# Optimization experiments

Hardware: AMD Instinct MI355X
Metric: run time of the kernel (lower is better)

Reference implementation:

```python
import jax, jax.numpy as jnp
import numpy as np

N_NODES = 100000
N_EDGES = 1600000
IN_DIM, HIDDEN, OUT = 128, 64, 32


def setup_inputs() -> dict:
    key = jax.random.key(0)
    k1, k2, k3, k4 = jax.random.split(key, 4)
    x = jax.random.normal(k1, (N_NODES, IN_DIM), dtype=jnp.float32)
    edge_index = jax.random.randint(k2, (2, N_EDGES), 0, N_NODES, dtype=jnp.int64)
    # Glorot-style init for GCN weights
    W1 = jax.random.normal(k3, (IN_DIM, HIDDEN), dtype=jnp.float32) / np.sqrt(IN_DIM)
    b1 = jnp.zeros((HIDDEN,), dtype=jnp.float32)
    W2 = jax.random.normal(k4, (HIDDEN, OUT), dtype=jnp.float32) / np.sqrt(HIDDEN)
    b2 = jnp.zeros((OUT,), dtype=jnp.float32)
    return {"x": x, "edge_index": edge_index, "W1": W1, "b1": b1, "W2": W2, "b2": b2}


def _gcn_conv(x, src, dst, W, b, n_nodes):
    """PyG GCNConv: h = W x; symmetric-normalized scatter-add over edges
    (self-loops already appended to src/dst)."""
    h = x @ W  # [N, F_out] — transform first (F_out <= F_in)
    ones = jnp.ones_like(dst, dtype=h.dtype)
    deg = jax.ops.segment_sum(ones, dst, num_segments=n_nodes)  # in-degree incl. self-loop
    dinv = jnp.where(deg > 0, jax.lax.rsqrt(deg), 0.0)
    norm = dinv[src] * dinv[dst]  # [E]
    msg = h[src] * norm[:, None]  # [E, F_out] — dominant gather
    agg = jax.ops.segment_sum(msg, dst, num_segments=n_nodes)  # [N, F_out]
    return agg + b


def reference(x, edge_index, W1, b1, W2, b2):
    n_nodes = x.shape[0]
    loops = jnp.arange(n_nodes, dtype=edge_index.dtype)
    src = jnp.concatenate([edge_index[0], loops])
    dst = jnp.concatenate([edge_index[1], loops])
    h = jax.nn.relu(_gcn_conv(x, src, dst, W1, b1, n_nodes))
    out = jax.nn.relu(_gcn_conv(h, src, dst, W2, b2, n_nodes))
    return out
```

## Files before the change

### kernel.cpp

```cpp
#include <hip/hip_runtime.h>

#define IN_DIM 128
#define HID    64
#define OUTD   32

#define BSHIFT 9
#define BNODES 512
#define NB     196
#define BCAP   16384
#define CHUNK  4096

#define XPAD   136

typedef __attribute__((ext_vector_type(8))) short bf16x8;
typedef __attribute__((ext_vector_type(4))) float f32x4;


__device__ __forceinline__ unsigned bfp2(float x, float y) {
    unsigned a = __float_as_uint(x); a = a + 0x7FFF + ((a >> 16) & 1);
    unsigned b = __float_as_uint(y); b = b + 0x7FFF + ((b >> 16) & 1);
    return (a >> 16) | (b & 0xFFFF0000u);
}

__device__ __forceinline__ unsigned short bf1(float x) {
    unsigned u = __float_as_uint(x);
    u += 0x7FFF + ((u >> 16) & 1);
    return (unsigned short)(u >> 16);
}

__device__ __forceinline__ void acc8(float* f, uint4 q) {
    f[0] += __uint_as_float(q.x << 16); f[1] += __uint_as_float(q.x & 0xFFFF0000u);
    f[2] += __uint_as_float(q.y << 16); f[3] += __uint_as_float(q.y & 0xFFFF0000u);
    f[4] += __uint_as_float(q.z << 16); f[5] += __uint_as_float(q.z & 0xFFFF0000u);
    f[6] += __uint_as_float(q.w << 16); f[7] += __uint_as_float(q.w & 0xFFFF0000u);
}


__global__ void k_binit(int* __restrict__ bucketCursor) {
    int t = threadIdx.x;
    if (t < NB) bucketCursor[t] = t * BCAP;
}


__launch_bounds__(256)
__global__ void k_bscatter(const int* __restrict__ src, const int* __restrict__ dst,
                           int* __restrict__ bucketCursor, int* __restrict__ ebuf, int E) {
    __shared__ int h[NB];
    __shared__ int lbase[NB];
    __shared__ int lcur[NB];
    const int t = threadIdx.x;
    const int base = blockIdx.x * CHUNK;
    const int nI4 = (min(CHUNK, E - base)) >> 2;
    const int4* d4 = (const int4*)(dst + base);
    const int4* s4 = (const int4*)(src + base);

    int4 dv0, dv1, dv2, dv3;
    const bool v0 = t < nI4, v1 = t + 256 < nI4, v2 = t + 512 < nI4, v3 = t + 768 < nI4;
    if (v0) dv0 = d4[t];
    if (v1) dv1 = d4[t + 256];
    if (v2) dv2 = d4[t + 512];
    if (v3) dv3 = d4[t + 768];

    for (int i = t; i < NB; i += 256) { h[i] = 0; lcur[i] = 0; }
    __syncthreads();

    if (v0) { atomicAdd(&h[dv0.x >> BSHIFT], 1); atomicAdd(&h[dv0.y >> BSHIFT], 1);
              atomicAdd(&h[dv0.z >> BSHIFT], 1); atomicAdd(&h[dv0.w >> BSHIFT], 1); }
    if (v1) { atomicAdd(&h[dv1.x >> BSHIFT], 1); atomicAdd(&h[dv1.y >> BSHIFT], 1);
              atomicAdd(&h[dv1.z >> BSHIFT], 1); atomicAdd(&h[dv1.w >> BSHIFT], 1); }
    if (v2) { atomicAdd(&h[dv2.x >> BSHIFT], 1); atomicAdd(&h[dv2.y >> BSHIFT], 1);
              atomicAdd(&h[dv2.z >> BSHIFT], 1); atomicAdd(&h[dv2.w >> BSHIFT], 1); }
    if (v3) { atomicAdd(&h[dv3.x >> BSHIFT], 1); atomicAdd(&h[dv3.y >> BSHIFT], 1);
              atomicAdd(&h[dv3.z >> BSHIFT], 1); atomicAdd(&h[dv3.w >> BSHIFT], 1); }
    __syncthreads();

    for (int i = t; i < NB; i += 256)
        lbase[i] = h[i] ? atomicAdd(&bucketCursor[i], h[i]) : 0;
    __syncthreads();

    #define SC1(D, S) { int b_ = (D) >> BSHIFT; int off_ = atomicAdd(&lcur[b_], 1); \
                        ebuf[lbase[b_] + off_] = ((S) << BSHIFT) | ((D) & (BNODES - 1)); }
    if (v0) { int4 sv = s4[t];       SC1(dv0.x, sv.x); SC1(dv0.y, sv.y); SC1(dv0.z, sv.z); SC1(dv0.w, sv.w); }
    if (v1) { int4 sv = s4[t + 256]; SC1(dv1.x, sv.x); SC1(dv1.y, sv.y); SC1(dv1.z, sv.z); SC1(dv1.w, sv.w); }
    if (v2) { int4 sv = s4[t + 512]; SC1(dv2.x, sv.x); SC1(dv2.y, sv.y); SC1(dv2.z, sv.z); SC1(dv2.w, sv.w); }
    if (v3) { int4 sv = s4[t + 768]; SC1(dv3.x, sv.x); SC1(dv3.y, sv.y); SC1(dv3.z, sv.z); SC1(dv3.w, sv.w); }
    #undef SC1
}


__launch_bounds__(256)
__global__ void k_bfinal(const int* __restrict__ ebuf, const int* __restrict__ bucketCursor,
                         int* __restrict__ rs, int* __restrict__ re, float* __restrict__ dinv,
                         int* __restrict__ csr, int N) {
    __shared__ int hist[BNODES];
    __shared__ int rsl[BNODES];
    __shared__ int ssum[256];
    const int t = threadIdx.x;
    const int b = blockIdx.x;
    const int nodeBase = b << BSHIFT;
    const int ebase = b * BCAP;
    const int cnt = bucketCursor[b] - ebase;
    const int nI4 = cnt >> 2;
    const int4* e4 = (const int4*)(ebuf + ebase);

    hist[t] = 0; hist[t + 256] = 0;
    __syncthreads();
    for (int i = t; i < nI4; i += 256) {
        int4 v = e4[i];
        atomicAdd(&hist[v.x & (BNODES - 1)], 1);
        atomicAdd(&hist[v.y & (BNODES - 1)], 1);
        atomicAdd(&hist[v.z & (BNODES - 1)], 1);
        atomicAdd(&hist[v.w & (BNODES - 1)], 1);
    }
    if (t < (cnt & 3))
        atomicAdd(&hist[ebuf[ebase + (nI4 << 2) + t] & (BNODES - 1)], 1);
    __syncthreads();

    int h0 = hist[2 * t], h1 = hist[2 * t + 1];
    ssum[t] = h0 + h1;
    __syncthreads();
    for (int off = 1; off < 256; off <<= 1) {
        int u = (t >= off) ? ssum[t - off] : 0;
        __syncthreads();
        ssum[t] += u;
        __syncthreads();
    }
    int excl = ssum[t] - h0 - h1;
    rsl[2 * t]     = excl;
    rsl[2 * t + 1] = excl + h0;

    int n0 = nodeBase + 2 * t, n1 = n0 + 1;
    if (n0 < N) {
        rs[n0] = ebase + excl;           re[n0] = ebase + excl + h0;
        dinv[n0] = rsqrtf((float)h0 + 1.0f);
    }
    if (n1 < N) {
        rs[n1] = ebase + excl + h0;      re[n1] = ebase + excl + h0 + h1;
        dinv[n1] = rsqrtf((float)h1 + 1.0f);
    }

    hist[2 * t] = 0; hist[2 * t + 1] = 0;
    __syncthreads();

    #define FILL1(P) { int l_ = (P) & (BNODES - 1); int off_ = atomicAdd(&hist[l_], 1); \
                       csr[ebase + rsl[l_] + off_] = ((unsigned)(P)) >> BSHIFT; }
    for (int i = t; i < nI4; i += 256) {
        int4 v = e4[i];
        FILL1(v.x); FILL1(v.y); FILL1(v.z); FILL1(v.w);
    }
    if (t < (cnt & 3))
        FILL1(ebuf[ebase + (nI4 << 2) + t]);
    #undef FILL1
}


__launch_bounds__(256)
__global__ void k_gemm1(const float* __restrict__ x, const float* __restrict__ W1,
                        const float* __restrict__ dinv, unsigned short* __restrict__ hs1b, int N) {
    __shared__ unsigned short xsb[64 * XPAD];
    __shared__ unsigned short wsb[64 * XPAD];
    const int t = threadIdx.x;
    const int base = blockIdx.x * 64;

    for (int i = t; i < IN_DIM * HID; i += 256) {
        int k = i >> 6, n = i & 63;
        wsb[n * XPAD + k] = bf1(W1[i]);
    }
    {
        const float4* s4 = (const float4*)(x + (size_t)base * IN_DIM);
        #pragma unroll
        for (int j = 0; j < 8; ++j) {
            int idx = t + j * 256;
            int r = idx >> 5, k4 = (idx & 31) * 4;
            ushort4 o;
            if (base + r < N) {
                float4 v = s4[idx];
                o.x = bf1(v.x); o.y = bf1(v.y); o.z = bf1(v.z); o.w = bf1(v.w);
            } else {
                o.x = 0; o.y = 0; o.z = 0; o.w = 0;
            }
            *(ushort4*)&xsb[r * XPAD + k4] = o;
        }
    }
    __syncthreads();

    const int lane = t & 63;
    const int w    = t >> 6;
    const int lr   = lane & 15;
    const int kg   = lane >> 4;

    f32x4 acc0 = {0,0,0,0}, acc1 = {0,0,0,0}, acc2 = {0,0,0,0}, acc3 = {0,0,0,0};
    #pragma unroll
    for (int kb = 0; kb < 4; ++kb) {
        int ko = kb * 32 + kg * 8;
        bf16x8 af = *(const bf16x8*)&xsb[(w * 16 + lr) * XPAD + ko];
        bf16x8 b0 = *(const bf16x8*)&wsb[( 0 + lr) * XPAD + ko];
        bf16x8 b1 = *(const bf16x8*)&wsb[(16 + lr) * XPAD + ko];
        bf16x8 b2 = *(const bf16x8*)&wsb[(32 + lr) * XPAD + ko];
        bf16x8 b3 = *(const bf16x8*)&wsb[(48 + lr) * XPAD + ko];
        acc0 = __builtin_amdgcn_mfma_f32_16x16x32_bf16(af, b0, acc0, 0, 0, 0);
        acc1 = __builtin_amdgcn_mfma_f32_16x16x32_bf16(af, b1, acc1, 0, 0, 0);
        acc2 = __builtin_amdgcn_mfma_f32_16x16x32_bf16(af, b2, acc2, 0, 0, 0);
        acc3 = __builtin_amdgcn_mfma_f32_16x16x32_bf16(af, b3, acc3, 0, 0, 0);
    }

    #pragma unroll
    for (int j = 0; j < 4; ++j) {
        int node = base + w * 16 + kg * 4 + j;
        if (node < N) {
            float d = dinv[node];
            unsigned short* o = hs1b + (size_t)node * HID + lr;
            o[0]  = bf1(acc0[j] * d);
            o[16] = bf1(acc1[j] * d);
            o[32] = bf1(acc2[j] * d);
            o[48] = bf1(acc3[j] * d);
        }
    }
}


__launch_bounds__(128)
__global__ void k_fuse2(const uint4* __restrict__ hs, const int* __restrict__ rs,
                        const int* __restrict__ re, const int* __restrict__ csr,
                        const float* __restrict__ dinv,
                        const float* __restrict__ b1, const float* __restrict__ W2,
                        uint2* __restrict__ hs2b, int N) {
    __shared__ float Ws[HID * OUTD];
    __shared__ float L1s[16 * 68];
    const int t = threadIdx.x;
    const int base = blockIdx.x * 16;

    for (int i = t; i < HID * OUTD / 4; i += 128)
        ((float4*)Ws)[i] = ((const float4*)W2)[i];

    {
        int node = base + (t >> 3);
        int lane = t & 7;
        float fa[8] = {0,0,0,0,0,0,0,0};
        float fb[8] = {0,0,0,0,0,0,0,0};
        float fc[8] = {0,0,0,0,0,0,0,0};
        float fd[8] = {0,0,0,0,0,0,0,0};
        acc8(fa, hs[(size_t)node * 8 + lane]);
        int i = rs[node];
        const int end = re[node];
        for (; i + 4 <= end; i += 4) {
            int s0 = __builtin_nontemporal_load(csr + i);
            int s1 = __builtin_nontemporal_load(csr + i + 1);
            int s2 = __builtin_nontemporal_load(csr + i + 2);
            int s3 = __builtin_nontemporal_load(csr + i + 3);
            uint4 q0 = hs[(size_t)s0 * 8 + lane];
            uint4 q1 = hs[(size_t)s1 * 8 + lane];
            uint4 q2 = hs[(size_t)s2 * 8 + lane];
            uint4 q3 = hs[(size_t)s3 * 8 + lane];
            acc8(fa, q0); acc8(fb, q1); acc8(fc, q2); acc8(fd, q3);
        }
        if (i + 2 <= end) {
            int s0 = __builtin_nontemporal_load(csr + i);
            int s1 = __builtin_nontemporal_load(csr + i + 1);
            uint4 q0 = hs[(size_t)s0 * 8 + lane];
            uint4 q1 = hs[(size_t)s1 * 8 + lane];
            acc8(fa, q0); acc8(fb, q1);
            i += 2;
        }
        if (i < end) {
            int s0 = __builtin_nontemporal_load(csr + i);
            acc8(fa, hs[(size_t)s0 * 8 + lane]);
        }
        float dn = dinv[node];
        const float4* bb4 = (const float4*)(b1 + lane * 8);
        float4 bv0 = bb4[0], bv1 = bb4[1];
        float* Lrow = &L1s[(t >> 3) * 68 + lane * 8];
        Lrow[0] = fmaxf((fa[0] + fb[0] + fc[0] + fd[0]) * dn + bv0.x, 0.0f);
        Lrow[1] = fmaxf((fa[1] + fb[1] + fc[1] + fd[1]) * dn + bv0.y, 0.0f);
        Lrow[2] = fmaxf((fa[2] + fb[2] + fc[2] + fd[2]) * dn + bv0.z, 0.0f);
        Lrow[3] = fmaxf((fa[3] + fb[3] + fc[3] + fd[3]) * dn + bv0.w, 0.0f);
        Lrow[4] = fmaxf((fa[4] + fb[4] + fc[4] + fd[4]) * dn + bv1.x, 0.0f);
        Lrow[5] = fmaxf((fa[5] + fb[5] + fc[5] + fd[5]) * dn + bv1.y, 0.0f);
        Lrow[6] = fmaxf((fa[6] + fb[6] + fc[6] + fd[6]) * dn + bv1.z, 0.0f);
        Lrow[7] = fmaxf((fa[7] + fb[7] + fc[7] + fd[7]) * dn + bv1.w, 0.0f);
    }
    __syncthreads();

    {
        const int fq = t & 7;
        const int nl = t >> 3;
        float4 a = {0,0,0,0};
        #pragma unroll 8
        for (int k = 0; k < HID; ++k) {
            float4 w = ((const float4*)Ws)[k * 8 + fq];
            float xv = L1s[nl * 68 + k];
            a.x += xv * w.x; a.y += xv * w.y; a.z += xv * w.z; a.w += xv * w.w;
        }
        int n = base + nl;
        float d = dinv[n];
        a.x *= d; a.y *= d; a.z *= d; a.w *= d;
        hs2b[(size_t)n * 8 + fq] = make_uint2(bfp2(a.x, a.y), bfp2(a.z, a.w));
    }
}


__launch_bounds__(128)
__global__ void k_agg2(const uint4* __restrict__ hs, const int* __restrict__ rs,
                       const int* __restrict__ re, const int* __restrict__ csr,
                       const float* __restrict__ dinv,
                       const float* __restrict__ b2, float* __restrict__ out, int N) {
    int tid = blockIdx.x * 128 + threadIdx.x;
    int node = tid >> 2;
    int lane = tid & 3;

    float fa[8] = {0,0,0,0,0,0,0,0};
    float fb[8] = {0,0,0,0,0,0,0,0};
    float fc[8] = {0,0,0,0,0,0,0,0};
    float fd[8] = {0,0,0,0,0,0,0,0};
    acc8(fa, hs[(size_t)node * 4 + lane]);
    int i = rs[node];
    const int end = re[node];
    for (; i + 4 <= end; i += 4) {
        int s0 = __builtin_nontemporal_load(csr + i);
        int s1 = __builtin_nontemporal_load(csr + i + 1);
        int s2 = __builtin_nontemporal_load(csr + i + 2);
        int s3 = __builtin_nontemporal_load(csr + i + 3);
        uint4 q0 = hs[(size_t)s0 * 4 + lane];
        uint4 q1 = hs[(size_t)s1 * 4 + lane];
        uint4 q2 = hs[(size_t)s2 * 4 + lane];
        uint4 q3 = hs[(size_t)s3 * 4 + lane];
        acc8(fa, q0); acc8(fb, q1); acc8(fc, q2); acc8(fd, q3);
    }
    if (i + 2 <= end) {
        int s0 = __builtin_nontemporal_load(csr + i);
        int s1 = __builtin_nontemporal_load(csr + i + 1);
        uint4 q0 = hs[(size_t)s0 * 4 + lane];
        uint4 q1 = hs[(size_t)s1 * 4 + lane];
        acc8(fa, q0); acc8(fb, q1);
        i += 2;
    }
    if (i < end) {
        int s0 = __builtin_nontemporal_load(csr + i);
        acc8(fa, hs[(size_t)s0 * 4 + lane]);
    }
    float dn = dinv[node];
    const float4* bb4 = (const float4*)(b2 + lane * 8);
    float4 b0 = bb4[0], b1v = bb4[1];
    float4 o0, o1;
    o0.x = fmaxf((fa[0] + fb[0] + fc[0] + fd[0]) * dn + b0.x, 0.0f);
    o0.y = fmaxf((fa[1] + fb[1] + fc[1] + fd[1]) * dn + b0.y, 0.0f);
    o0.z = fmaxf((fa[2] + fb[2] + fc[2] + fd[2]) * dn + b0.z, 0.0f);
    o0.w = fmaxf((fa[3] + fb[3] + fc[3] + fd[3]) * dn + b0.w, 0.0f);
    o1.x = fmaxf((fa[4] + fb[4] + fc[4] + fd[4]) * dn + b1v.x, 0.0f);
    o1.y = fmaxf((fa[5] + fb[5] + fc[5] + fd[5]) * dn + b1v.y, 0.0f);
    o1.z = fmaxf((fa[6] + fb[6] + fc[6] + fd[6]) * dn + b1v.z, 0.0f);
    o1.w = fmaxf((fa[7] + fb[7] + fc[7] + fd[7]) * dn + b1v.w, 0.0f);
    float4* o = (float4*)(out + (size_t)node * OUTD + lane * 8);
    o[0] = o0;
    o[1] = o1;
}


extern "C" void kernel_launch(void* const* d_in, const int* in_sizes, int n_in,
                              void* d_out, int out_size, void* d_ws, size_t ws_size,
                              hipStream_t stream) {
    const float* x  = (const float*)d_in[0];
    const int*   ei = (const int*)  d_in[1];
    const float* W1 = (const float*)d_in[2];
    const float* b1 = (const float*)d_in[3];
    const float* W2 = (const float*)d_in[4];
    const float* b2 = (const float*)d_in[5];

    const int N = in_sizes[0] / IN_DIM;
    const int E = in_sizes[1] / 2;
    const int* srcI = ei;
    const int* dstI = ei + E;
    float* out = (float*)d_out;

    float* dinv         = (float*)d_ws;
    int*   rs           = (int*)d_ws + 131072;
    int*   re           = (int*)d_ws + 2 * 131072;
    int*   bucketCursor = (int*)d_ws + 3 * 131072;
    int*   ebuf         = (int*)d_ws + 4 * 131072;
    int*   csr          = ebuf + (size_t)NB * BCAP;
    uint2* hs1b         = (uint2*)(csr + (size_t)NB * BCAP);
    uint2* hs2b         = hs1b + (size_t)N * 16;

    k_binit   <<<1, 256, 0, stream>>>(bucketCursor);
    k_bscatter<<<(E + CHUNK - 1) / CHUNK, 256, 0, stream>>>(srcI, dstI, bucketCursor, ebuf, E);
    k_bfinal  <<<NB, 256, 0, stream>>>(ebuf, bucketCursor, rs, re, dinv, csr, N);

    k_gemm1<<<(N + 63) / 64, 256, 0, stream>>>(x, W1, dinv, (unsigned short*)hs1b, N);
    k_fuse2<<<N / 16, 128, 0, stream>>>((const uint4*)hs1b, rs, re, csr, dinv, b1, W2, hs2b, N);
    k_agg2 <<<N / 32, 128, 0, stream>>>((const uint4*)hs2b, rs, re, csr, dinv, b2, out, N);
}
```

Before: 128.2 us.

## Co-schedule layer-1 GEMM with edge bucket scatter in one launch

The first-layer GEMM no longer depends on dinv, so it is merged into the bucket-scatter kernel as extra blocks, letting the dense transform overlap with the edge bucketing. The source-side normalization moves into the layer-1 aggregation, which now gathers dinv[src] per edge and uses an FMA instead of an add. The intent is to remove a dependent launch and hide GEMM time behind the atomic-heavy scatter. In exchange, each edge costs an extra random 4-byte gather, and the merged kernel's larger shared-memory footprint may lower occupancy for the scatter blocks.

```diff
diff --git a/kernel.cpp b/kernel.cpp
--- a/kernel.cpp
+++ b/kernel.cpp
@@ -35,6 +35,17 @@
     f[6] += __uint_as_float(q.w << 16); f[7] += __uint_as_float(q.w & 0xFFFF0000u);
 }
 
+__device__ __forceinline__ void facc8(float* f, uint4 q, float s) {
+    f[0] = fmaf(__uint_as_float(q.x << 16),          s, f[0]);
+    f[1] = fmaf(__uint_as_float(q.x & 0xFFFF0000u),  s, f[1]);
+    f[2] = fmaf(__uint_as_float(q.y << 16),          s, f[2]);
+    f[3] = fmaf(__uint_as_float(q.y & 0xFFFF0000u),  s, f[3]);
+    f[4] = fmaf(__uint_as_float(q.z << 16),          s, f[4]);
+    f[5] = fmaf(__uint_as_float(q.z & 0xFFFF0000u),  s, f[5]);
+    f[6] = fmaf(__uint_as_float(q.w << 16),          s, f[6]);
+    f[7] = fmaf(__uint_as_float(q.w & 0xFFFF0000u),  s, f[7]);
+}
+
 
 __global__ void k_binit(int* __restrict__ bucketCursor) {
     int t = threadIdx.x;
@@ -43,48 +54,111 @@
 
 
 __launch_bounds__(256)
-__global__ void k_bscatter(const int* __restrict__ src, const int* __restrict__ dst,
-                           int* __restrict__ bucketCursor, int* __restrict__ ebuf, int E) {
+__global__ void k_bsg(const int* __restrict__ src, const int* __restrict__ dst,
+                      int* __restrict__ bucketCursor, int* __restrict__ ebuf, int E, int nBsc,
+                      const float* __restrict__ x, const float* __restrict__ W1,
+                      unsigned short* __restrict__ hs1b, int N) {
     __shared__ int h[NB];
     __shared__ int lbase[NB];
     __shared__ int lcur[NB];
+    __shared__ unsigned short xsb[64 * XPAD];
+    __shared__ unsigned short wsb[64 * XPAD];
     const int t = threadIdx.x;
-    const int base = blockIdx.x * CHUNK;
-    const int nI4 = (min(CHUNK, E - base)) >> 2;
-    const int4* d4 = (const int4*)(dst + base);
-    const int4* s4 = (const int4*)(src + base);
-
-    int4 dv0, dv1, dv2, dv3;
-    const bool v0 = t < nI4, v1 = t + 256 < nI4, v2 = t + 512 < nI4, v3 = t + 768 < nI4;
-    if (v0) dv0 = d4[t];
-    if (v1) dv1 = d4[t + 256];
-    if (v2) dv2 = d4[t + 512];
-    if (v3) dv3 = d4[t + 768];
-
-    for (int i = t; i < NB; i += 256) { h[i] = 0; lcur[i] = 0; }
-    __syncthreads();
-
-    if (v0) { atomicAdd(&h[dv0.x >> BSHIFT], 1); atomicAdd(&h[dv0.y >> BSHIFT], 1);
-              atomicAdd(&h[dv0.z >> BSHIFT], 1); atomicAdd(&h[dv0.w >> BSHIFT], 1); }
-    if (v1) { atomicAdd(&h[dv1.x >> BSHIFT], 1); atomicAdd(&h[dv1.y >> BSHIFT], 1);
-              atomicAdd(&h[dv1.z >> BSHIFT], 1); atomicAdd(&h[dv1.w >> BSHIFT], 1); }
-    if (v2) { atomicAdd(&h[dv2.x >> BSHIFT], 1); atomicAdd(&h[dv2.y >> BSHIFT], 1);
-              atomicAdd(&h[dv2.z >> BSHIFT], 1); atomicAdd(&h[dv2.w >> BSHIFT], 1); }
-    if (v3) { atomicAdd(&h[dv3.x >> BSHIFT], 1); atomicAdd(&h[dv3.y >> BSHIFT], 1);
-              atomicAdd(&h[dv3.z >> BSHIFT], 1); atomicAdd(&h[dv3.w >> BSHIFT], 1); }
-    __syncthreads();
-
-    for (int i = t; i < NB; i += 256)
-        lbase[i] = h[i] ? atomicAdd(&bucketCursor[i], h[i]) : 0;
-    __syncthreads();
-
-    #define SC1(D, S) { int b_ = (D) >> BSHIFT; int off_ = atomicAdd(&lcur[b_], 1); \
-                        ebuf[lbase[b_] + off_] = ((S) << BSHIFT) | ((D) & (BNODES - 1)); }
-    if (v0) { int4 sv = s4[t];       SC1(dv0.x, sv.x); SC1(dv0.y, sv.y); SC1(dv0.z, sv.z); SC1(dv0.w, sv.w); }
-    if (v1) { int4 sv = s4[t + 256]; SC1(dv1.x, sv.x); SC1(dv1.y, sv.y); SC1(dv1.z, sv.z); SC1(dv1.w, sv.w); }
-    if (v2) { int4 sv = s4[t + 512]; SC1(dv2.x, sv.x); SC1(dv2.y, sv.y); SC1(dv2.z, sv.z); SC1(dv2.w, sv.w); }
-    if (v3) { int4 sv = s4[t + 768]; SC1(dv3.x, sv.x); SC1(dv3.y, sv.y); SC1(dv3.z, sv.z); SC1(dv3.w, sv.w); }
-    #undef SC1
+
+    if ((int)blockIdx.x < nBsc) {
+        const int base = blockIdx.x * CHUNK;
+        const int nI4 = (min(CHUNK, E - base)) >> 2;
+        const int4* d4 = (const int4*)(dst + base);
+        const int4* s4 = (const int4*)(src + base);
+
+        int4 dv0, dv1, dv2, dv3;
+        const bool v0 = t < nI4, v1 = t + 256 < nI4, v2 = t + 512 < nI4, v3 = t + 768 < nI4;
+        if (v0) dv0 = d4[t];
+        if (v1) dv1 = d4[t + 256];
+        if (v2) dv2 = d4[t + 512];
+        if (v3) dv3 = d4[t + 768];
+
+        for (int i = t; i < NB; i += 256) { h[i] = 0; lcur[i] = 0; }
+        __syncthreads();
+
+        if (v0) { atomicAdd(&h[dv0.x >> BSHIFT], 1); atomicAdd(&h[dv0.y >> BSHIFT], 1);
+                  atomicAdd(&h[dv0.z >> BSHIFT], 1); atomicAdd(&h[dv0.w >> BSHIFT], 1); }
+        if (v1) { atomicAdd(&h[dv1.x >> BSHIFT], 1); atomicAdd(&h[dv1.y >> BSHIFT], 1);
+                  atomicAdd(&h[dv1.z >> BSHIFT], 1); atomicAdd(&h[dv1.w >> BSHIFT], 1); }
+        if (v2) { atomicAdd(&h[dv2.x >> BSHIFT], 1); atomicAdd(&h[dv2.y >> BSHIFT], 1);
+                  atomicAdd(&h[dv2.z >> BSHIFT], 1); atomicAdd(&h[dv2.w >> BSHIFT], 1); }
+        if (v3) { atomicAdd(&h[dv3.x >> BSHIFT], 1); atomicAdd(&h[dv3.y >> BSHIFT], 1);
+                  atomicAdd(&h[dv3.z >> BSHIFT], 1); atomicAdd(&h[dv3.w >> BSHIFT], 1); }
+        __syncthreads();
+
+        for (int i = t; i < NB; i += 256)
+            lbase[i] = h[i] ? atomicAdd(&bucketCursor[i], h[i]) : 0;
+        __syncthreads();
+
+        #define SC1(D, S) { int b_ = (D) >> BSHIFT; int off_ = atomicAdd(&lcur[b_], 1); \
+                            ebuf[lbase[b_] + off_] = ((S) << BSHIFT) | ((D) & (BNODES - 1)); }
+        if (v0) { int4 sv = s4[t];       SC1(dv0.x, sv.x); SC1(dv0.y, sv.y); SC1(dv0.z, sv.z); SC1(dv0.w, sv.w); }
+        if (v1) { int4 sv = s4[t + 256]; SC1(dv1.x, sv.x); SC1(dv1.y, sv.y); SC1(dv1.z, sv.z); SC1(dv1.w, sv.w); }
+        if (v2) { int4 sv = s4[t + 512]; SC1(dv2.x, sv.x); SC1(dv2.y, sv.y); SC1(dv2.z, sv.z); SC1(dv2.w, sv.w); }
+        if (v3) { int4 sv = s4[t + 768]; SC1(dv3.x, sv.x); SC1(dv3.y, sv.y); SC1(dv3.z, sv.z); SC1(dv3.w, sv.w); }
+        #undef SC1
+    } else {
+        const int base = ((int)blockIdx.x - nBsc) * 64;
+
+        for (int i = t; i < IN_DIM * HID; i += 256) {
+            int k = i >> 6, n = i & 63;
+            wsb[n * XPAD + k] = bf1(W1[i]);
+        }
+        {
+            const float4* s4 = (const float4*)(x + (size_t)base * IN_DIM);
+            #pragma unroll
+            for (int j = 0; j < 8; ++j) {
+                int idx = t + j * 256;
+                int r = idx >> 5, k4 = (idx & 31) * 4;
+                ushort4 o;
+                if (base + r < N) {
+                    float4 v = s4[idx];
+                    o.x = bf1(v.x); o.y = bf1(v.y); o.z = bf1(v.z); o.w = bf1(v.w);
+                } else {
+                    o.x = 0; o.y = 0; o.z = 0; o.w = 0;
+                }
+                *(ushort4*)&xsb[r * XPAD + k4] = o;
+            }
+        }
+        __syncthreads();
+
+        const int lane = t & 63;
+        const int w    = t >> 6;
+        const int lr   = lane & 15;
+        const int kg   = lane >> 4;
+
+        f32x4 acc0 = {0,0,0,0}, acc1 = {0,0,0,0}, acc2 = {0,0,0,0}, acc3 = {0,0,0,0};
+        #pragma unroll
+        for (int kb = 0; kb < 4; ++kb) {
+            int ko = kb * 32 + kg * 8;
+            bf16x8 af = *(const bf16x8*)&xsb[(w * 16 + lr) * XPAD + ko];
+            bf16x8 b0 = *(const bf16x8*)&wsb[( 0 + lr) * XPAD + ko];
+            bf16x8 b1 = *(const bf16x8*)&wsb[(16 + lr) * XPAD + ko];
+            bf16x8 b2 = *(const bf16x8*)&wsb[(32 + lr) * XPAD + ko];
+            bf16x8 b3 = *(const bf16x8*)&wsb[(48 + lr) * XPAD + ko];
+            acc0 = __builtin_amdgcn_mfma_f32_16x16x32_bf16(af, b0, acc0, 0, 0, 0);
+            acc1 = __builtin_amdgcn_mfma_f32_16x16x32_bf16(af, b1, acc1, 0, 0, 0);
+            acc2 = __builtin_amdgcn_mfma_f32_16x16x32_bf16(af, b2, acc2, 0, 0, 0);
+            acc3 = __builtin_amdgcn_mfma_f32_16x16x32_bf16(af, b3, acc3, 0, 0, 0);
+        }
+
+        #pragma unroll
+        for (int j = 0; j < 4; ++j) {
+            int node = base + w * 16 + kg * 4 + j;
+            if (node < N) {
+                unsigned short* o = hs1b + (size_t)node * HID + lr;
+                o[0]  = bf1(acc0[j]);
+                o[16] = bf1(acc1[j]);
+                o[32] = bf1(acc2[j]);
+                o[48] = bf1(acc3[j]);
+            }
+        }
+    }
 }
 
 
@@ -154,71 +228,6 @@
 }
 
 
-__launch_bounds__(256)
-__global__ void k_gemm1(const float* __restrict__ x, const float* __restrict__ W1,
-                        const float* __restrict__ dinv, unsigned short* __restrict__ hs1b, int N) {
-    __shared__ unsigned short xsb[64 * XPAD];
-    __shared__ unsigned short wsb[64 * XPAD];
-    const int t = threadIdx.x;
-    const int base = blockIdx.x * 64;
-
-    for (int i = t; i < IN_DIM * HID; i += 256) {
-        int k = i >> 6, n = i & 63;
-        wsb[n * XPAD + k] = bf1(W1[i]);
-    }
-    {
-        const float4* s4 = (const float4*)(x + (size_t)base * IN_DIM);
-        #pragma unroll
-        for (int j = 0; j < 8; ++j) {
-            int idx = t + j * 256;
-            int r = idx >> 5, k4 = (idx & 31) * 4;
-            ushort4 o;
-            if (base + r < N) {
-                float4 v = s4[idx];
-                o.x = bf1(v.x); o.y = bf1(v.y); o.z = bf1(v.z); o.w = bf1(v.w);
-            } else {
-                o.x = 0; o.y = 0; o.z = 0; o.w = 0;
-            }
-            *(ushort4*)&xsb[r * XPAD + k4] = o;
-        }
-    }
-    __syncthreads();
-
-    const int lane = t & 63;
-    const int w    = t >> 6;
-    const int lr   = lane & 15;
-    const int kg   = lane >> 4;
-
-    f32x4 acc0 = {0,0,0,0}, acc1 = {0,0,0,0}, acc2 = {0,0,0,0}, acc3 = {0,0,0,0};
-    #pragma unroll
-    for (int kb = 0; kb < 4; ++kb) {
-        int ko = kb * 32 + kg * 8;
-        bf16x8 af = *(const bf16x8*)&xsb[(w * 16 + lr) * XPAD + ko];
-        bf16x8 b0 = *(const bf16x8*)&wsb[( 0 + lr) * XPAD + ko];
-        bf16x8 b1 = *(const bf16x8*)&wsb[(16 + lr) * XPAD + ko];
-        bf16x8 b2 = *(const bf16x8*)&wsb[(32 + lr) * XPAD + ko];
-        bf16x8 b3 = *(const bf16x8*)&wsb[(48 + lr) * XPAD + ko];
-        acc0 = __builtin_amdgcn_mfma_f32_16x16x32_bf16(af, b0, acc0, 0, 0, 0);
-        acc1 = __builtin_amdgcn_mfma_f32_16x16x32_bf16(af, b1, acc1, 0, 0, 0);
-        acc2 = __builtin_amdgcn_mfma_f32_16x16x32_bf16(af, b2, acc2, 0, 0, 0);
-        acc3 = __builtin_amdgcn_mfma_f32_16x16x32_bf16(af, b3, acc3, 0, 0, 0);
-    }
-
-    #pragma unroll
-    for (int j = 0; j < 4; ++j) {
-        int node = base + w * 16 + kg * 4 + j;
-        if (node < N) {
-            float d = dinv[node];
-            unsigned short* o = hs1b + (size_t)node * HID + lr;
-            o[0]  = bf1(acc0[j] * d);
-            o[16] = bf1(acc1[j] * d);
-            o[32] = bf1(acc2[j] * d);
-            o[48] = bf1(acc3[j] * d);
-        }
-    }
-}
-
-
 __launch_bounds__(128)
 __global__ void k_fuse2(const uint4* __restrict__ hs, const int* __restrict__ rs,
                         const int* __restrict__ re, const int* __restrict__ csr,
@@ -236,11 +245,12 @@
     {
         int node = base + (t >> 3);
         int lane = t & 7;
+        float dn = dinv[node];
         float fa[8] = {0,0,0,0,0,0,0,0};
         float fb[8] = {0,0,0,0,0,0,0,0};
         float fc[8] = {0,0,0,0,0,0,0,0};
         float fd[8] = {0,0,0,0,0,0,0,0};
-        acc8(fa, hs[(size_t)node * 8 + lane]);
+        facc8(fa, hs[(size_t)node * 8 + lane], dn);
         int i = rs[node];
         const int end = re[node];
         for (; i + 4 <= end; i += 4) {
@@ -248,25 +258,26 @@
             int s1 = __builtin_nontemporal_load(csr + i + 1);
             int s2 = __builtin_nontemporal_load(csr + i + 2);
             int s3 = __builtin_nontemporal_load(csr + i + 3);
+            float d0 = dinv[s0], d1 = dinv[s1], d2 = dinv[s2], d3 = dinv[s3];
             uint4 q0 = hs[(size_t)s0 * 8 + lane];
             uint4 q1 = hs[(size_t)s1 * 8 + lane];
             uint4 q2 = hs[(size_t)s2 * 8 + lane];
             uint4 q3 = hs[(size_t)s3 * 8 + lane];
-            acc8(fa, q0); acc8(fb, q1); acc8(fc, q2); acc8(fd, q3);
+            facc8(fa, q0, d0); facc8(fb, q1, d1); facc8(fc, q2, d2); facc8(fd, q3, d3);
         }
         if (i + 2 <= end) {
             int s0 = __builtin_nontemporal_load(csr + i);
             int s1 = __builtin_nontemporal_load(csr + i + 1);
+            float d0 = dinv[s0], d1 = dinv[s1];
             uint4 q0 = hs[(size_t)s0 * 8 + lane];
             uint4 q1 = hs[(size_t)s1 * 8 + lane];
-            acc8(fa, q0); acc8(fb, q1);
+            facc8(fa, q0, d0); facc8(fb, q1, d1);
             i += 2;
         }
         if (i < end) {
             int s0 = __builtin_nontemporal_load(csr + i);
-            acc8(fa, hs[(size_t)s0 * 8 + lane]);
-        }
-        float dn = dinv[node];
+            facc8(fa, hs[(size_t)s0 * 8 + lane], dinv[s0]);
+        }
         const float4* bb4 = (const float4*)(b1 + lane * 8);
         float4 bv0 = bb4[0], bv1 = bb4[1];
         float* Lrow = &L1s[(t >> 3) * 68 + lane * 8];
@@ -381,11 +392,14 @@
     uint2* hs1b         = (uint2*)(csr + (size_t)NB * BCAP);
     uint2* hs2b         = hs1b + (size_t)N * 16;
 
-    k_binit   <<<1, 256, 0, stream>>>(bucketCursor);
-    k_bscatter<<<(E + CHUNK - 1) / CHUNK, 256, 0, stream>>>(srcI, dstI, bucketCursor, ebuf, E);
-    k_bfinal  <<<NB, 256, 0, stream>>>(ebuf, bucketCursor, rs, re, dinv, csr, N);
-
-    k_gemm1<<<(N + 63) / 64, 256, 0, stream>>>(x, W1, dinv, (unsigned short*)hs1b, N);
+    const int nBsc = (E + CHUNK - 1) / CHUNK;
+    const int nG1  = (N + 63) / 64;
+
+    k_binit <<<1, 256, 0, stream>>>(bucketCursor);
+    k_bsg   <<<nBsc + nG1, 256, 0, stream>>>(srcI, dstI, bucketCursor, ebuf, E, nBsc,
+                                             x, W1, (unsigned short*)hs1b, N);
+    k_bfinal<<<NB, 256, 0, stream>>>(ebuf, bucketCursor, rs, re, dinv, csr, N);
+
     k_fuse2<<<N / 16, 128, 0, stream>>>((const uint4*)hs1b, rs, re, csr, dinv, b1, W2, hs2b, N);
     k_agg2 <<<N / 32, 128, 0, stream>>>((const uint4*)hs2b, rs, re, csr, dinv, b2, out, N);
 }
```

New measurement: 125.4 us. 1.02x faster.
